# Performance work log

Measured on AMD Instinct MI355X. Metric: run time of the kernel, lower is better.

Reference implementation:

```python
import jax, jax.numpy as jnp
import numpy as np

# Grid / problem sizes (match init_kwargs)
B, D, H, W = 2, 64, 256, 256      # batch + spatial_shape
N = 524288                         # active voxels
IN_DIM, HID = 32, 32               # input_dim, hidden_dim
C_IN = IN_DIM + HID                # conv in-channels (64)
C_OUT = 4 * HID                    # conv out-channels (128)
OFFSETS = [(dz, dy, dx) for dz in (-1, 0, 1) for dy in (-1, 0, 1) for dx in (-1, 0, 1)]


def setup_inputs() -> dict:
    key = jax.random.key(0)
    ks = jax.random.split(key, 5)
    # Unique active-voxel coordinates: odd multiplier is a bijection mod 2^k grid size.
    total = B * D * H * W
    MULT = 2654435761  # odd => injective on arange(N) mod total (total is a power of 2)
    lin = (np.arange(N, dtype=np.int64) * MULT) % total
    b = lin // (D * H * W)
    r = lin % (D * H * W)
    z = r // (H * W)
    r = r % (H * W)
    y = r // W
    x = r % W
    coors = jnp.asarray(np.stack([b, z, y, x], axis=1).astype(np.int32))  # [N,4]
    x_features = jax.random.normal(ks[0], (N, IN_DIM), jnp.float32)
    h_features = jax.random.normal(ks[1], (N, HID), jnp.float32)
    c_features = jax.random.normal(ks[2], (N, HID), jnp.float32)
    weight = jax.random.normal(ks[3], (27, C_IN, C_OUT), jnp.float32) * 0.05
    bias = jax.random.normal(ks[4], (C_OUT,), jnp.float32) * 0.05
    return {"x_features": x_features, "h_features": h_features,
            "c_features": c_features, "weight": weight, "bias": bias,
            "coors": coors, "batch_size": B}


def _subm_conv3d(feats, weight, bias, coors):
    """Submanifold sparse 3x3x3 conv: output only at active sites;
    gather-GEMM-scatter via a dense coordinate->point-id map (the rulebook)."""
    b, z, y, x = coors[:, 0], coors[:, 1], coors[:, 2], coors[:, 3]
    pid = jnp.arange(N, dtype=jnp.int32)
    idx_map = jnp.full((B, D, H, W), -1, jnp.int32).at[b, z, y, x].set(pid)
    out = jnp.zeros((N, C_OUT), feats.dtype) + bias  # [N, 4*HID]
    for k, (dz, dy, dx) in enumerate(OFFSETS):
        nz, ny, nx = z + dz, y + dy, x + dx
        inb = (nz >= 0) & (nz < D) & (ny >= 0) & (ny < H) & (nx >= 0) & (nx < W)
        nid = idx_map[b, jnp.clip(nz, 0, D - 1), jnp.clip(ny, 0, H - 1), jnp.clip(nx, 0, W - 1)]
        nid = jnp.where(inb, nid, -1)
        valid = nid >= 0
        gathered = jnp.where(valid[:, None], feats[jnp.maximum(nid, 0)], 0.0)  # [N, C_IN]
        out = out + gathered @ weight[k]
    return out


def reference(x_features, h_features, c_features, weight, bias, coors, batch_size):
    combined = jnp.concatenate([x_features, h_features], axis=1)  # [N, C_IN]
    cc = _subm_conv3d(combined, weight, bias, coors)              # [N, 4*HID]
    cc_i, cc_f, cc_o, cc_g = jnp.split(cc, 4, axis=1)
    i = jax.nn.sigmoid(cc_i)
    f = jax.nn.sigmoid(cc_f)
    o = jax.nn.sigmoid(cc_o)
    g = jnp.tanh(cc_g)
    c_next = f * c_features + i * g
    h_next = o * jnp.tanh(c_next)
    return (h_next, c_next)
```

## Files before the change

### kernel.cpp

```cpp
#include <hip/hip_runtime.h>
#include <stdint.h>

#define N_PTS 524288
#define DQ 64
#define HQ 256
#define WQ 256
#define MAP_BYTES (2*DQ*HQ*WQ*4)
#define NBKT 4096

typedef short bf8  __attribute__((ext_vector_type(8)));
typedef float f16v __attribute__((ext_vector_type(16)));

static __device__ __forceinline__ short f2bf(float f) {
    union { float f; uint32_t u; } v; v.f = f;
    return (short)((v.u + 0x7fffu + ((v.u >> 16) & 1u)) >> 16);
}
static __device__ __forceinline__ float fast_sigmoid(float x) {
    return 1.f / (1.f + __expf(-x));
}
static __device__ __forceinline__ float fast_tanh(float x) {
    return 1.f - 2.f / (__expf(2.f * x) + 1.f);
}

__global__ void k_feats(const float* __restrict__ xf, const float* __restrict__ hf,
                        const int* __restrict__ coors, int* __restrict__ hist,
                        short* __restrict__ fb, int* __restrict__ map) {
    int t = blockIdx.x * 256 + threadIdx.x;
    int n = t >> 3, seg = t & 7;
    const float* src = (seg < 4) ? (xf + n*32 + seg*8) : (hf + n*32 + seg*8 - 32);
    float4 a = ((const float4*)src)[0];
    float4 b = ((const float4*)src)[1];
    bf8 rv;
    rv[0]=f2bf(a.x); rv[1]=f2bf(a.y); rv[2]=f2bf(a.z); rv[3]=f2bf(a.w);
    rv[4]=f2bf(b.x); rv[5]=f2bf(b.y); rv[6]=f2bf(b.z); rv[7]=f2bf(b.w);
    ((bf8*)fb)[t] = rv;
    if (seg == 0) {
        int4 c = ((const int4*)coors)[n];
        int mb = ((c.x*DQ + c.y)*HQ + c.z)*WQ + c.w;
        map[mb] = n;
        atomicAdd(&hist[mb >> 11], 1);
    }
}

__global__ void k_scan(int* __restrict__ hist) {
    __shared__ int wsum[4];
    int tid = threadIdx.x;
    int lane = tid & 63, wv = tid >> 6;
    int v[16]; int s = 0;
    #pragma unroll
    for (int i = 0; i < 16; i++) { v[i] = hist[tid*16 + i]; s += v[i]; }
    int sc = s;
    #pragma unroll
    for (int d = 1; d < 64; d <<= 1) {
        int t = __shfl_up(sc, d, 64);
        if (lane >= d) sc += t;
    }
    if (lane == 63) wsum[wv] = sc;
    __syncthreads();
    int base = 0;
    #pragma unroll
    for (int w = 0; w < 4; w++) if (w < wv) base += wsum[w];
    int excl = base + sc - s;
    #pragma unroll
    for (int i = 0; i < 16; i++) { int c = v[i]; hist[tid*16 + i] = excl; excl += c; }
}

__global__ void k_rank(const int* __restrict__ coors, int* __restrict__ hist,
                       int* __restrict__ sorg) {
    int n = blockIdx.x * 256 + threadIdx.x;
    int4 c = ((const int4*)coors)[n];
    int mb = ((c.x*DQ + c.y)*HQ + c.z)*WQ + c.w;
    int slot = atomicAdd(&hist[mb >> 11], 1);
    sorg[slot] = n;
}

__global__ void k_wt(const float* __restrict__ w, short* __restrict__ wt) {
    int t = blockIdx.x * 256 + threadIdx.x;
    if (t >= 27*64*128) return;
    int jj = t & 7, c = (t >> 3) & 127, jg = (t >> 10) & 7, k = t >> 13;
    int j = jg*8 + jj;
    wt[t] = f2bf(w[(k*64 + j)*128 + c]);
}

__launch_bounds__(256, 2)
__global__ void k_main(const int* __restrict__ map, const short* __restrict__ fb,
                       const short* __restrict__ wt, const float* __restrict__ bias,
                       const float* __restrict__ cfeat, const int* __restrict__ coors,
                       const int* __restrict__ sorg, const short* __restrict__ zp,
                       float* __restrict__ out)
{
    __shared__ short Wlds[2][8192];

    const int tid  = threadIdx.x;
    const int lane = tid & 63;
    const int wv   = tid >> 6;
    const int l31  = lane & 31;
    const int lhi  = lane >> 5;

    const int bid   = (blockIdx.x & 7) * 256 + (blockIdx.x >> 3);
    const int pbase = bid * 256;
    const int p     = pbase + wv*64 + lane;

    const int orig = sorg[p];
    const int4 cr = ((const int4*)coors)[orig];
    const int mbase_zyx = cr.x*DQ + cr.y;

    auto probe = [&](int ko) -> int {
        int dz = ko/9 - 1, dy = (ko/3)%3 - 1, dxo = ko%3 - 1;
        int nz = cr.y + dz, ny = cr.z + dy, nx = cr.w + dxo;
        bool inb = ((unsigned)nz < (unsigned)DQ) & ((unsigned)ny < (unsigned)HQ) &
                   ((unsigned)nx < (unsigned)WQ);
        int cz = min(max(nz, 0), DQ-1);
        int cy = min(max(ny, 0), HQ-1);
        int cx = min(max(nx, 0), WQ-1);
        int nid = map[((cr.x*DQ + cz)*HQ + cy)*WQ + cx];
        return inb ? nid : -1;
    };

    auto stageW = [&](int ko) {
        const short* src = wt + ko*8192;
        #pragma unroll
        for (int i = 0; i < 4; i++) {
            int cb = i*256 + wv*64;
            __builtin_amdgcn_global_load_lds(
                (const __attribute__((address_space(1))) void*)(src + (size_t)(cb + lane)*8),
                (__attribute__((address_space(3))) void*)&Wlds[ko & 1][cb*8],
                16, 0, 0);
        }
    };

    auto gather = [&](int n0, int n1, bf8* dst) {
        const short* s0 = (n0 >= 0) ? (fb + (size_t)n0*64 + lhi*8) : (zp + lhi*8);
        const short* s1 = (n1 >= 0) ? (fb + (size_t)n1*64 + lhi*8) : (zp + lhi*8);
        #pragma unroll
        for (int j = 0; j < 4; j++) {
            dst[j]     = *(const bf8*)(s0 + j*16);
            dst[4 + j] = *(const bf8*)(s1 + j*16);
        }
    };

    f16v acc[2][4];
    #pragma unroll
    for (int mt = 0; mt < 2; mt++)
        #pragma unroll
        for (int ct = 0; ct < 4; ct++) {
            float bv = bias[ct*32 + l31];
            #pragma unroll
            for (int r = 0; r < 16; r++) acc[mt][ct][r] = bv;
        }

    stageW(0);
    int pA = probe(0);
    int pB = probe(1);
    int pr_old = probe(2);

    bf8 a_cur[8], a_next[8];
    {
        int g0 = __shfl(pA, l31, 64);
        int g1 = __shfl(pA, l31 + 32, 64);
        gather(g0, g1, a_cur);
    }
    int g0n = __shfl(pB, l31, 64);
    int g1n = __shfl(pB, l31 + 32, 64);

    __builtin_amdgcn_sched_barrier(0);
    asm volatile("s_waitcnt vmcnt(0)" ::: "memory");
    __builtin_amdgcn_s_barrier();

    #pragma unroll 1
    for (int ko = 0; ko < 27; ko++) {
        if (ko < 26) {
            stageW(ko + 1);
            __builtin_amdgcn_sched_barrier(0);
            gather(g0n, g1n, a_next);
        }
        int pr_new = (ko < 24) ? probe(ko + 3) : -1;

        const int buf = ko & 1;
        #pragma unroll
        for (int ks = 0; ks < 4; ks++) {
            int jg = ks*2 + lhi;
            const short* wb = &Wlds[buf][(jg*128 + l31)*8];
            #pragma unroll
            for (int ct = 0; ct < 4; ct++) {
                bf8 b = *(const bf8*)(wb + ct*32*8);
                acc[0][ct] = __builtin_amdgcn_mfma_f32_32x32x16_bf16(a_cur[ks],     b, acc[0][ct], 0, 0, 0);
                acc[1][ct] = __builtin_amdgcn_mfma_f32_32x32x16_bf16(a_cur[4 + ks], b, acc[1][ct], 0, 0, 0);
            }
        }

        if (ko < 25) {
            g0n = __shfl(pr_old, l31, 64);
            g1n = __shfl(pr_old, l31 + 32, 64);
            pr_old = pr_new;
        }
        #pragma unroll
        for (int j = 0; j < 8; j++) a_cur[j] = a_next[j];

        if (ko < 26) {
            __builtin_amdgcn_sched_barrier(0);
            if (ko < 24) { asm volatile("s_waitcnt vmcnt(9)" ::: "memory"); }
            else         { asm volatile("s_waitcnt vmcnt(8)" ::: "memory"); }
            __builtin_amdgcn_s_barrier();
        }
    }

    #pragma unroll
    for (int mt = 0; mt < 2; mt++) {
        #pragma unroll
        for (int r = 0; r < 16; r++) {
            int row = (r & 3) + 8*(r >> 2) + 4*lhi;
            int pp  = pbase + wv*64 + mt*32 + row;
            int opp = sorg[pp];
            float gi = acc[mt][0][r];
            float gf = acc[mt][1][r];
            float go = acc[mt][2][r];
            float gg = acc[mt][3][r];
            float cv = cfeat[opp*32 + l31];
            float si = fast_sigmoid(gi);
            float sf = fast_sigmoid(gf);
            float so = fast_sigmoid(go);
            float tg = fast_tanh(gg);
            float cn = sf*cv + si*tg;
            float hn = so * fast_tanh(cn);
            out[opp*32 + l31] = hn;
            out[N_PTS*32 + opp*32 + l31] = cn;
        }
    }
}

extern "C" void kernel_launch(void* const* d_in, const int* in_sizes, int n_in,
                              void* d_out, int out_size, void* d_ws, size_t ws_size,
                              hipStream_t stream) {
    const float* xf    = (const float*)d_in[0];
    const float* hf    = (const float*)d_in[1];
    const float* cf    = (const float*)d_in[2];
    const float* w     = (const float*)d_in[3];
    const float* bias  = (const float*)d_in[4];
    const int*   coors = (const int*)d_in[5];
    float* out = (float*)d_out;

    char* base = (char*)d_ws;
    int*   map    = (int*)base;
    short* fb     = (short*)(base + MAP_BYTES);
    short* wtb    = (short*)(base + 100663296);
    short* zp     = (short*)(base + 101105664);
    int*   sorg   = (int*)(base + 101106176);
    int*   hist   = (int*)(base + 103203328);

    hipMemsetAsync(map, 0xFF, MAP_BYTES, stream);
    hipMemsetAsync(hist, 0, NBKT*4, stream);
    hipMemsetAsync(zp, 0, 256, stream);
    k_feats<<<(N_PTS*8)/256, 256, 0, stream>>>(xf, hf, coors, hist, fb, map);
    k_scan<<<1, 256, 0, stream>>>(hist);
    k_rank<<<N_PTS/256, 256, 0, stream>>>(coors, hist, sorg);
    k_wt<<<(27*64*128 + 255)/256, 256, 0, stream>>>(w, wtb);
    k_main<<<N_PTS/256, 256, 0, stream>>>(map, fb, wtb, bias, cf, coors, sorg, zp, out);
}
```

Baseline: 568.2 us.

## Store features in sorted order and shrink main kernel tile to 32 points per wave

The preprocessing is reordered as histogram, scan, then a feature-conversion kernel that assigns each point its sorted slot. The map then stores sorted indices and the bf16 features are written in sorted order, so neighbour gathers in the main kernel hit spatially local rows. The main kernel now processes 32 points per wave instead of 64, halving accumulator registers so launch bounds can be raised to 3 blocks per CU. Probes are split across lane halves to cover two offsets at once. In exchange, weight tiles are reloaded from LDS for half as many rows, so weight staging per point doubles and there are twice as many blocks.

Measured after the change: 570.1 us. No clear change (+0.3%).

```diff
diff --git a/kernel.cpp b/kernel.cpp
--- a/kernel.cpp
+++ b/kernel.cpp
@@ -22,56 +22,59 @@
     return 1.f - 2.f / (__expf(2.f * x) + 1.f);
 }
 
+__global__ void k_hist(const int* __restrict__ coors, int* __restrict__ hist) {
+    int n = blockIdx.x * 256 + threadIdx.x;
+    int4 c = ((const int4*)coors)[n];
+    int mbase = ((c.x*DQ + c.y)*HQ + c.z)*WQ + c.w;
+    atomicAdd(&hist[mbase >> 11], 1);
+}
+
+__global__ void k_scan(int* __restrict__ hist) {
+    __shared__ int wsum[4];
+    int tid = threadIdx.x;
+    int lane = tid & 63, wv = tid >> 6;
+    int v[16]; int s = 0;
+    #pragma unroll
+    for (int i = 0; i < 16; i++) { v[i] = hist[tid*16 + i]; s += v[i]; }
+    int sc = s;
+    #pragma unroll
+    for (int d = 1; d < 64; d <<= 1) {
+        int t = __shfl_up(sc, d, 64);
+        if (lane >= d) sc += t;
+    }
+    if (lane == 63) wsum[wv] = sc;
+    __syncthreads();
+    int base = 0;
+    #pragma unroll
+    for (int w = 0; w < 4; w++) if (w < wv) base += wsum[w];
+    int excl = base + sc - s;
+    #pragma unroll
+    for (int i = 0; i < 16; i++) { int c = v[i]; hist[tid*16 + i] = excl; excl += c; }
+}
+
 __global__ void k_feats(const float* __restrict__ xf, const float* __restrict__ hf,
                         const int* __restrict__ coors, int* __restrict__ hist,
-                        short* __restrict__ fb, int* __restrict__ map) {
+                        short* __restrict__ fb, int* __restrict__ map,
+                        int* __restrict__ sorg) {
     int t = blockIdx.x * 256 + threadIdx.x;
     int n = t >> 3, seg = t & 7;
+    int lane = threadIdx.x & 63;
+    int slot = 0;
+    if (seg == 0) {
+        int4 c = ((const int4*)coors)[n];
+        int mb = ((c.x*DQ + c.y)*HQ + c.z)*WQ + c.w;
+        slot = atomicAdd(&hist[mb >> 11], 1);
+        map[mb] = slot;
+        sorg[slot] = n;
+    }
+    slot = __shfl(slot, lane & 56, 64);
     const float* src = (seg < 4) ? (xf + n*32 + seg*8) : (hf + n*32 + seg*8 - 32);
     float4 a = ((const float4*)src)[0];
     float4 b = ((const float4*)src)[1];
     bf8 rv;
     rv[0]=f2bf(a.x); rv[1]=f2bf(a.y); rv[2]=f2bf(a.z); rv[3]=f2bf(a.w);
     rv[4]=f2bf(b.x); rv[5]=f2bf(b.y); rv[6]=f2bf(b.z); rv[7]=f2bf(b.w);
-    ((bf8*)fb)[t] = rv;
-    if (seg == 0) {
-        int4 c = ((const int4*)coors)[n];
-        int mb = ((c.x*DQ + c.y)*HQ + c.z)*WQ + c.w;
-        map[mb] = n;
-        atomicAdd(&hist[mb >> 11], 1);
-    }
-}
-
-__global__ void k_scan(int* __restrict__ hist) {
-    __shared__ int wsum[4];
-    int tid = threadIdx.x;
-    int lane = tid & 63, wv = tid >> 6;
-    int v[16]; int s = 0;
-    #pragma unroll
-    for (int i = 0; i < 16; i++) { v[i] = hist[tid*16 + i]; s += v[i]; }
-    int sc = s;
-    #pragma unroll
-    for (int d = 1; d < 64; d <<= 1) {
-        int t = __shfl_up(sc, d, 64);
-        if (lane >= d) sc += t;
-    }
-    if (lane == 63) wsum[wv] = sc;
-    __syncthreads();
-    int base = 0;
-    #pragma unroll
-    for (int w = 0; w < 4; w++) if (w < wv) base += wsum[w];
-    int excl = base + sc - s;
-    #pragma unroll
-    for (int i = 0; i < 16; i++) { int c = v[i]; hist[tid*16 + i] = excl; excl += c; }
-}
-
-__global__ void k_rank(const int* __restrict__ coors, int* __restrict__ hist,
-                       int* __restrict__ sorg) {
-    int n = blockIdx.x * 256 + threadIdx.x;
-    int4 c = ((const int4*)coors)[n];
-    int mb = ((c.x*DQ + c.y)*HQ + c.z)*WQ + c.w;
-    int slot = atomicAdd(&hist[mb >> 11], 1);
-    sorg[slot] = n;
+    ((bf8*)fb)[slot*8 + seg] = rv;
 }
 
 __global__ void k_wt(const float* __restrict__ w, short* __restrict__ wt) {
@@ -82,7 +85,7 @@
     wt[t] = f2bf(w[(k*64 + j)*128 + c]);
 }
 
-__launch_bounds__(256, 2)
+__launch_bounds__(256, 3)
 __global__ void k_main(const int* __restrict__ map, const short* __restrict__ fb,
                        const short* __restrict__ wt, const float* __restrict__ bias,
                        const float* __restrict__ cfeat, const int* __restrict__ coors,
@@ -97,16 +100,15 @@
     const int l31  = lane & 31;
     const int lhi  = lane >> 5;
 
-    const int bid   = (blockIdx.x & 7) * 256 + (blockIdx.x >> 3);
-    const int pbase = bid * 256;
-    const int p     = pbase + wv*64 + lane;
-
-    const int orig = sorg[p];
+    const int bid   = (blockIdx.x & 7) * 512 + (blockIdx.x >> 3);
+    const int pw    = bid * 128 + wv * 32;
+
+    const int orig = sorg[pw + l31];
     const int4 cr = ((const int4*)coors)[orig];
-    const int mbase_zyx = cr.x*DQ + cr.y;
-
-    auto probe = [&](int ko) -> int {
-        int dz = ko/9 - 1, dy = (ko/3)%3 - 1, dxo = ko%3 - 1;
+
+    auto probe2 = [&](int o) -> int {
+        int oo = o + lhi;
+        int dz = oo/9 - 1, dy = (oo/3)%3 - 1, dxo = oo%3 - 1;
         int nz = cr.y + dz, ny = cr.z + dy, nx = cr.w + dxo;
         bool inb = ((unsigned)nz < (unsigned)DQ) & ((unsigned)ny < (unsigned)HQ) &
                    ((unsigned)nx < (unsigned)WQ);
@@ -129,52 +131,44 @@
         }
     };
 
-    auto gather = [&](int n0, int n1, bf8* dst) {
+    auto gather = [&](int n0, bf8* dst) {
         const short* s0 = (n0 >= 0) ? (fb + (size_t)n0*64 + lhi*8) : (zp + lhi*8);
-        const short* s1 = (n1 >= 0) ? (fb + (size_t)n1*64 + lhi*8) : (zp + lhi*8);
-        #pragma unroll
-        for (int j = 0; j < 4; j++) {
-            dst[j]     = *(const bf8*)(s0 + j*16);
-            dst[4 + j] = *(const bf8*)(s1 + j*16);
-        }
+        #pragma unroll
+        for (int ks = 0; ks < 4; ks++) dst[ks] = *(const bf8*)(s0 + ks*16);
     };
 
-    f16v acc[2][4];
-    #pragma unroll
-    for (int mt = 0; mt < 2; mt++)
-        #pragma unroll
-        for (int ct = 0; ct < 4; ct++) {
-            float bv = bias[ct*32 + l31];
-            #pragma unroll
-            for (int r = 0; r < 16; r++) acc[mt][ct][r] = bv;
-        }
+    f16v acc[4];
+    #pragma unroll
+    for (int ct = 0; ct < 4; ct++) {
+        float bv = bias[ct*32 + l31];
+        #pragma unroll
+        for (int r = 0; r < 16; r++) acc[ct][r] = bv;
+    }
 
     stageW(0);
-    int pA = probe(0);
-    int pB = probe(1);
-    int pr_old = probe(2);
-
-    bf8 a_cur[8], a_next[8];
-    {
-        int g0 = __shfl(pA, l31, 64);
-        int g1 = __shfl(pA, l31 + 32, 64);
-        gather(g0, g1, a_cur);
-    }
-    int g0n = __shfl(pB, l31, 64);
-    int g1n = __shfl(pB, l31 + 32, 64);
+    int pr01 = probe2(0);
+    int prm2 = probe2(2);
+    int prm1 = probe2(3);
+
+    bf8 a_cur[4], a_next[4];
+    gather(__shfl(pr01, l31, 64), a_cur);
+    int g0n = __shfl(pr01, l31 + 32, 64);
 
     __builtin_amdgcn_sched_barrier(0);
     asm volatile("s_waitcnt vmcnt(0)" ::: "memory");
     __builtin_amdgcn_s_barrier();
+    __builtin_amdgcn_sched_barrier(0);
 
     #pragma unroll 1
     for (int ko = 0; ko < 27; ko++) {
+        int pr0 = 0;
         if (ko < 26) {
             stageW(ko + 1);
             __builtin_amdgcn_sched_barrier(0);
-            gather(g0n, g1n, a_next);
-        }
-        int pr_new = (ko < 24) ? probe(ko + 3) : -1;
+            gather(g0n, a_next);
+            __builtin_amdgcn_sched_barrier(0);
+            pr0 = probe2(ko + 4);
+        }
 
         const int buf = ko & 1;
         #pragma unroll
@@ -184,48 +178,40 @@
             #pragma unroll
             for (int ct = 0; ct < 4; ct++) {
                 bf8 b = *(const bf8*)(wb + ct*32*8);
-                acc[0][ct] = __builtin_amdgcn_mfma_f32_32x32x16_bf16(a_cur[ks],     b, acc[0][ct], 0, 0, 0);
-                acc[1][ct] = __builtin_amdgcn_mfma_f32_32x32x16_bf16(a_cur[4 + ks], b, acc[1][ct], 0, 0, 0);
+                acc[ct] = __builtin_amdgcn_mfma_f32_32x32x16_bf16(a_cur[ks], b, acc[ct], 0, 0, 0);
             }
         }
 
-        if (ko < 25) {
-            g0n = __shfl(pr_old, l31, 64);
-            g1n = __shfl(pr_old, l31 + 32, 64);
-            pr_old = pr_new;
-        }
-        #pragma unroll
-        for (int j = 0; j < 8; j++) a_cur[j] = a_next[j];
+        if (ko < 25) g0n = __shfl(prm2, l31, 64);
+        prm2 = prm1; prm1 = pr0;
+        #pragma unroll
+        for (int j = 0; j < 4; j++) a_cur[j] = a_next[j];
 
         if (ko < 26) {
             __builtin_amdgcn_sched_barrier(0);
-            if (ko < 24) { asm volatile("s_waitcnt vmcnt(9)" ::: "memory"); }
-            else         { asm volatile("s_waitcnt vmcnt(8)" ::: "memory"); }
+            asm volatile("s_waitcnt vmcnt(5)" ::: "memory");
             __builtin_amdgcn_s_barrier();
-        }
-    }
-
-    #pragma unroll
-    for (int mt = 0; mt < 2; mt++) {
-        #pragma unroll
-        for (int r = 0; r < 16; r++) {
-            int row = (r & 3) + 8*(r >> 2) + 4*lhi;
-            int pp  = pbase + wv*64 + mt*32 + row;
-            int opp = sorg[pp];
-            float gi = acc[mt][0][r];
-            float gf = acc[mt][1][r];
-            float go = acc[mt][2][r];
-            float gg = acc[mt][3][r];
-            float cv = cfeat[opp*32 + l31];
-            float si = fast_sigmoid(gi);
-            float sf = fast_sigmoid(gf);
-            float so = fast_sigmoid(go);
-            float tg = fast_tanh(gg);
-            float cn = sf*cv + si*tg;
-            float hn = so * fast_tanh(cn);
-            out[opp*32 + l31] = hn;
-            out[N_PTS*32 + opp*32 + l31] = cn;
-        }
+            __builtin_amdgcn_sched_barrier(0);
+        }
+    }
+
+    #pragma unroll
+    for (int r = 0; r < 16; r++) {
+        int row = (r & 3) + 8*(r >> 2) + 4*lhi;
+        int opp = __shfl(orig, row, 64);
+        float gi = acc[0][r];
+        float gf = acc[1][r];
+        float go = acc[2][r];
+        float gg = acc[3][r];
+        float cv = cfeat[opp*32 + l31];
+        float si = fast_sigmoid(gi);
+        float sf = fast_sigmoid(gf);
+        float so = fast_sigmoid(go);
+        float tg = fast_tanh(gg);
+        float cn = sf*cv + si*tg;
+        float hn = so * fast_tanh(cn);
+        out[opp*32 + l31] = hn;
+        out[N_PTS*32 + opp*32 + l31] = cn;
     }
 }
 
@@ -251,9 +237,9 @@
     hipMemsetAsync(map, 0xFF, MAP_BYTES, stream);
     hipMemsetAsync(hist, 0, NBKT*4, stream);
     hipMemsetAsync(zp, 0, 256, stream);
-    k_feats<<<(N_PTS*8)/256, 256, 0, stream>>>(xf, hf, coors, hist, fb, map);
+    k_hist<<<N_PTS/256, 256, 0, stream>>>(coors, hist);
     k_scan<<<1, 256, 0, stream>>>(hist);
-    k_rank<<<N_PTS/256, 256, 0, stream>>>(coors, hist, sorg);
+    k_feats<<<(N_PTS*8)/256, 256, 0, stream>>>(xf, hf, coors, hist, fb, map, sorg);
     k_wt<<<(27*64*128 + 255)/256, 256, 0, stream>>>(w, wtb);
-    k_main<<<N_PTS/256, 256, 0, stream>>>(map, fb, wtb, bias, cf, coors, sorg, zp, out);
-}
+    k_main<<<N_PTS/128, 256, 0, stream>>>(map, fb, wtb, bias, cf, coors, sorg, zp, out);
+}
```
